# Optimization experiments

Hardware: AMD Instinct MI355X
Metric: run time of the kernel (lower is better)

The kernel has to match this reference:

```python
import jax, jax.numpy as jnp
import numpy as np

N_NODES = 50000
NUM_FEA = 213
HID, IN_HEAD = 16, 12
OUT_DIM, OUT_HEAD = 8, 8
NEG_SLOPE = 0.2


def gat_conv(x, W, att_src, att_dst, bias, src, dst, H, C):
    # x: [N, F] -> h: [N, H, C]
    N = x.shape[0]
    h = (x @ W).reshape(N, H, C)
    a_s = jnp.sum(h * att_src, axis=-1)  # [N, H]
    a_d = jnp.sum(h * att_dst, axis=-1)  # [N, H]
    e = jax.nn.leaky_relu(a_s[src] + a_d[dst], NEG_SLOPE)  # [E, H]
    # segment softmax over incoming edges of each dst node
    m = jax.ops.segment_max(e, dst, num_segments=N)
    ex = jnp.exp(e - m[dst])
    denom = jax.ops.segment_sum(ex, dst, num_segments=N)
    alpha = ex / denom[dst]  # [E, H]
    out = jax.ops.segment_sum(h[src] * alpha[:, :, None], dst, num_segments=N)
    return out.reshape(N, H * C) + bias


def setup_inputs() -> dict:
    key = jax.random.key(0)
    ks = jax.random.split(key, 16)
    E = 800000
    P = 16384
    features = jax.random.normal(ks[0], (N_NODES, NUM_FEA), dtype=jnp.float32)
    edge_index = jax.random.randint(ks[1], (2, E), 0, N_NODES, dtype=jnp.int32)
    node1_index = jax.random.randint(ks[2], (P,), 0, N_NODES, dtype=jnp.int32)
    node2_index = jax.random.randint(ks[3], (P,), 0, N_NODES, dtype=jnp.int32)
    s1 = 1.0 / np.sqrt(NUM_FEA)
    s2 = 1.0 / np.sqrt(HID * IN_HEAD)
    s3 = 1.0 / np.sqrt(OUT_DIM * OUT_HEAD * 2)
    params = {
        'W1': jax.random.normal(ks[4], (NUM_FEA, IN_HEAD * HID), jnp.float32) * s1,
        'att_src1': jax.random.normal(ks[5], (IN_HEAD, HID), jnp.float32) * s1,
        'att_dst1': jax.random.normal(ks[6], (IN_HEAD, HID), jnp.float32) * s1,
        'b1': jnp.zeros((IN_HEAD * HID,), jnp.float32),
        'W2': jax.random.normal(ks[7], (IN_HEAD * HID, OUT_HEAD * OUT_DIM), jnp.float32) * s2,
        'att_src2': jax.random.normal(ks[8], (OUT_HEAD, OUT_DIM), jnp.float32) * s2,
        'att_dst2': jax.random.normal(ks[9], (OUT_HEAD, OUT_DIM), jnp.float32) * s2,
        'b2': jnp.zeros((OUT_HEAD * OUT_DIM,), jnp.float32),
        'linW': jax.random.normal(ks[10], (OUT_DIM * OUT_HEAD * 2, 2), jnp.float32) * s3,
        'linb': jnp.zeros((2,), jnp.float32),
    }
    return dict(features=features, edge_index=edge_index,
                node1_index=node1_index, node2_index=node2_index, **params)


def reference(features, edge_index, node1_index, node2_index,
              W1, att_src1, att_dst1, b1, W2, att_src2, att_dst2, b2, linW, linb):
    # eval mode: dropout(p=0.8) is identity
    N = features.shape[0]
    self_loops = jnp.arange(N, dtype=edge_index.dtype)
    src = jnp.concatenate([edge_index[0], self_loops])
    dst = jnp.concatenate([edge_index[1], self_loops])
    x = gat_conv(features, W1, att_src1, att_dst1, b1, src, dst, IN_HEAD, HID)
    x = jax.nn.elu(x)
    x = gat_conv(x, W2, att_src2, att_dst2, b2, src, dst, OUT_HEAD, OUT_DIM)
    x = jax.nn.elu(x)
    pair = jnp.concatenate([x[node1_index], x[node2_index]], axis=1)
    y_pred = jax.nn.sigmoid(pair @ linW + linb)
    return (y_pred, x)
```

## Files before the change

### kernel.cpp

```cpp
#include <hip/hip_runtime.h>
#include <hip/hip_bf16.h>

#define HID1 16
#define NHEAD1 12
#define F1 (HID1*NHEAD1)
#define HID2 8
#define NHEAD2 8
#define F2 (HID2*NHEAD2)
#define NUM_FEA 213
#define NEG_SLOPE 0.2f
#define KP 224
#define KP2 192
#define LDK 40
#define MR1 64
#define MROWS 128
#define NC1 224
#define NW2R 80
#define SLOTS 56
#define BINS 256
#define NPB 196
#define CAP 4096
#define FILLB 256
#define EPT 13

typedef __attribute__((ext_vector_type(8))) __bf16 bf16x8;
typedef __attribute__((ext_vector_type(4))) float floatx4;
typedef __attribute__((ext_vector_type(2))) float floatx2;
typedef float floatx4u __attribute__((ext_vector_type(4), aligned(4)));
typedef unsigned short ushort_t;

static __device__ __forceinline__ unsigned short f2bf(float f) {
    unsigned u = __float_as_uint(f);
    unsigned r = (u + 0x7fffu + ((u >> 16) & 1u)) >> 16;
    return (unsigned short)r;
}
static __device__ __forceinline__ float lrelu(float e) {
    return e > 0.f ? e : NEG_SLOPE * e;
}
static __device__ __forceinline__ float elu(float v) {
    return v > 0.f ? v : (__expf(v) - 1.f);
}


__global__ __launch_bounds__(256) void prep_kernel(
        const float* __restrict__ W1, const float* __restrict__ as1w,
        const float* __restrict__ ad1w, ushort_t* __restrict__ Wt1,
        const float* __restrict__ W2, const float* __restrict__ as2w,
        const float* __restrict__ ad2w, ushort_t* __restrict__ Wt2,
        const int* __restrict__ ei, int* __restrict__ binctr,
        unsigned* __restrict__ binbuf, int E, int Etot, int nwb) {
    int b = (int)blockIdx.x;
    int tid = threadIdx.x;
    if (b >= nwb) {
        __shared__ int hist[BINS];
        __shared__ int cur[BINS];
        int fb = b - nwb;
        if (tid < BINS) hist[tid] = 0;
        __syncthreads();
        unsigned stash[EPT];
        int base_e = fb * 256 + tid;
#pragma unroll
        for (int i = 0; i < EPT; i++) {
            int e = base_e + i * (FILLB * 256);
            unsigned pk = 0xffffffffu;
            if (e < Etot) {
                int s, d;
                if (e < E) { s = ei[e]; d = ei[E + e]; } else { s = e - E; d = s; }
                pk = (unsigned)s | ((unsigned)d << 16);
                atomicAdd(&hist[(unsigned)d / NPB], 1);
            }
            stash[i] = pk;
        }
        __syncthreads();
        if (tid < BINS) cur[tid] = atomicAdd(&binctr[tid], hist[tid]);
        __syncthreads();
#pragma unroll
        for (int i = 0; i < EPT; i++) {
            unsigned pk = stash[i];
            if (pk != 0xffffffffu) {
                int d = (int)(pk >> 16);
                int bin = (int)((unsigned)d / NPB);
                int dl = d - bin * NPB;
                int r = atomicAdd(&cur[bin], 1);
                if (r < CAP)
                    binbuf[(long)bin * CAP + r] = (pk & 0xffffu) | ((unsigned)dl << 16);
            }
        }
        return;
    }
    int j = b * 256 + tid;
    if (j < NC1 * KP) {
        int n = j / KP, k = j - n * KP;
        float v = 0.f;
        if (k < NUM_FEA) {
            if (n < 192) {
                v = W1[(long)k * F1 + n];
            } else if (n < 204) {
                int hd = n - 192;
                for (int c = 0; c < HID1; c++)
                    v += W1[(long)k * F1 + hd * HID1 + c] * as1w[hd * HID1 + c];
            } else if (n < 216) {
                int hd = n - 204;
                for (int c = 0; c < HID1; c++)
                    v += W1[(long)k * F1 + hd * HID1 + c] * ad1w[hd * HID1 + c];
            }
        }
        Wt1[j] = f2bf(v);
    } else {
        int j2 = j - NC1 * KP;
        if (j2 < NW2R * KP2) {
            int n = j2 / KP2, k = j2 - n * KP2;
            float v;
            if (n < 64) {
                v = W2[(long)k * F2 + n];
            } else if (n < 72) {
                int hd = n - 64;
                v = 0.f;
                for (int c = 0; c < HID2; c++)
                    v += W2[(long)k * F2 + hd * HID2 + c] * as2w[hd * HID2 + c];
            } else {
                int hd = n - 72;
                v = 0.f;
                for (int c = 0; c < HID2; c++)
                    v += W2[(long)k * F2 + hd * HID2 + c] * ad2w[hd * HID2 + c];
            }
            Wt2[j2] = f2bf(v);
        }
    }
}


static __device__ __forceinline__ void stageA(ushort_t* dst, const float* xp,
                                              bool ok, int col) {
    union { int4 q; ushort_t u[8]; } pk;
    if (ok && col + 8 <= NUM_FEA) {
        floatx4u a = *(const floatx4u*)(xp + col);
        floatx4u c = *(const floatx4u*)(xp + col + 4);
#pragma unroll
        for (int j = 0; j < 4; j++) { pk.u[j] = f2bf(a[j]); pk.u[4 + j] = f2bf(c[j]); }
    } else {
#pragma unroll
        for (int j = 0; j < 8; j++) {
            float v = (ok && col + j < NUM_FEA) ? xp[col + j] : 0.f;
            pk.u[j] = f2bf(v);
        }
    }
    *(int4*)dst = pk.q;
}

__global__ __launch_bounds__(256) void gemm1_bs_kernel(
        const float* __restrict__ X, const ushort_t* __restrict__ Wt,
        ushort_t* __restrict__ Hout, float* __restrict__ as_, float* __restrict__ ad_,
        const unsigned* __restrict__ binbuf, const int* __restrict__ binctr,
        ushort_t* __restrict__ esrcp, int* __restrict__ cnt,
        int N, int nblk_gemm) {
    __shared__ ushort_t As[MR1 * LDK];
    __shared__ ushort_t Bs[NC1 * LDK];
    __shared__ int lcnt[NPB];
    int tid = threadIdx.x;
    if ((int)blockIdx.x >= nblk_gemm) {
        int b = (int)blockIdx.x - nblk_gemm;
        if (tid < NPB) lcnt[tid] = 0;
        __syncthreads();
        int cntb = binctr[b];
        if (cntb > CAP) cntb = CAP;
        const unsigned* seg = binbuf + (long)b * CAP;
        for (int t = tid; t < cntb; t += 256) {
            unsigned u = seg[t];
            int s = (int)(u & 0xffffu);
            int dl = (int)(u >> 16);
            int slot = atomicAdd(&lcnt[dl], 1);
            if (slot < SLOTS)
                esrcp[(long)(b * NPB + dl) * SLOTS + slot] = (ushort_t)s;
        }
        __syncthreads();
        int d = b * NPB + tid;
        if (tid < NPB && d < N) cnt[d] = lcnt[tid];
        return;
    }
    int wave = tid >> 6, lane = tid & 63;
    int q = lane >> 4, l16 = lane & 15;
    int wm = (wave >> 1) * 32;
    int wn = (wave & 1) * 112;
    long row0 = (long)blockIdx.x * MR1;

    int r0 = tid >> 2, ksl = (tid & 3) * 8;
    long gr0 = row0 + r0;
    bool ok0 = gr0 < N;
    const float* xp0 = X + gr0 * NUM_FEA;
    ushort_t* lds0 = &As[r0 * LDK + ksl];

    floatx4 acc[2][7] = {};

    for (int k0 = 0; k0 < KP; k0 += 32) {
        stageA(lds0, xp0, ok0, k0 + ksl);
#pragma unroll
        for (int p = 0; p < 4; p++) {
            int idx = p * 256 + tid;
            if (idx < NC1 * 4) {
                int r = idx >> 2, ks = (idx & 3) * 8;
                *(int4*)&Bs[r * LDK + ks] = *(const int4*)&Wt[(long)r * KP + k0 + ks];
            }
        }
        __syncthreads();
        bf16x8 af[2], bfr[7];
#pragma unroll
        for (int rt = 0; rt < 2; rt++)
            af[rt] = *(const bf16x8*)&As[(wm + rt * 16 + l16) * LDK + q * 8];
#pragma unroll
        for (int ct = 0; ct < 7; ct++)
            bfr[ct] = *(const bf16x8*)&Bs[(wn + ct * 16 + l16) * LDK + q * 8];
#pragma unroll
        for (int rt = 0; rt < 2; rt++)
#pragma unroll
            for (int ct = 0; ct < 7; ct++)
                acc[rt][ct] = __builtin_amdgcn_mfma_f32_16x16x32_bf16(af[rt], bfr[ct], acc[rt][ct], 0, 0, 0);
        __syncthreads();
    }
#pragma unroll
    for (int rt = 0; rt < 2; rt++) {
#pragma unroll
        for (int r = 0; r < 4; r++) {
            long grow = row0 + wm + rt * 16 + q * 4 + r;
            if (grow < N) {
#pragma unroll
                for (int ct = 0; ct < 7; ct++) {
                    int col = wn + ct * 16 + l16;
                    float v = acc[rt][ct][r];
                    if (col < 192)      Hout[grow * F1 + col] = f2bf(v);
                    else if (col < 204) as_[grow * NHEAD1 + col - 192] = v;
                    else if (col < 216) ad_[grow * NHEAD1 + col - 204] = v;
                }
            }
        }
    }
}


__global__ __launch_bounds__(256) void gemm2_mfma(const ushort_t* __restrict__ Xbf,
                                                  const ushort_t* __restrict__ Wt,
                                                  ushort_t* __restrict__ Hout,
                                                  float* __restrict__ as_,
                                                  float* __restrict__ ad_, int N) {
    __shared__ ushort_t As[MROWS * LDK];
    __shared__ ushort_t Bs[96 * LDK];
    int tid = threadIdx.x;
    int wave = tid >> 6, lane = tid & 63;
    int q = lane >> 4, l16 = lane & 15;
    int wm = (wave >> 1) * 64;
    int wn = (wave & 1) * 48;
    long row0 = (long)blockIdx.x * MROWS;

    floatx4 acc[4][3] = {};

    for (int k0 = 0; k0 < KP2; k0 += 32) {
#pragma unroll
        for (int p = 0; p < 2; p++) {
            int idx = p * 256 + tid;
            int r = idx >> 2, ks = (idx & 3) * 8;
            *(int4*)&As[r * LDK + ks] = *(const int4*)&Xbf[(row0 + r) * KP2 + k0 + ks];
        }
#pragma unroll
        for (int p = 0; p < 2; p++) {
            int idx = p * 256 + tid;
            if (idx < 96 * 4) {
                int r = idx >> 2, ks = (idx & 3) * 8;
                int4 z = {0, 0, 0, 0};
                *(int4*)&Bs[r * LDK + ks] = (r < NW2R) ? *(const int4*)&Wt[(long)r * KP2 + k0 + ks] : z;
            }
        }
        __syncthreads();
        bf16x8 af[4], bfr[3];
#pragma unroll
        for (int rt = 0; rt < 4; rt++)
            af[rt] = *(const bf16x8*)&As[(wm + rt * 16 + l16) * LDK + q * 8];
#pragma unroll
        for (int ct = 0; ct < 3; ct++)
            bfr[ct] = *(const bf16x8*)&Bs[(wn + ct * 16 + l16) * LDK + q * 8];
#pragma unroll
        for (int rt = 0; rt < 4; rt++)
#pragma unroll
            for (int ct = 0; ct < 3; ct++)
                acc[rt][ct] = __builtin_amdgcn_mfma_f32_16x16x32_bf16(af[rt], bfr[ct], acc[rt][ct], 0, 0, 0);
        __syncthreads();
    }
#pragma unroll
    for (int rt = 0; rt < 4; rt++) {
#pragma unroll
        for (int r = 0; r < 4; r++) {
            long grow = row0 + wm + rt * 16 + q * 4 + r;
            if (grow < N) {
#pragma unroll
                for (int ct = 0; ct < 3; ct++) {
                    int col = wn + ct * 16 + l16;
                    float v = acc[rt][ct][r];
                    if (col < 64)      Hout[grow * F2 + col] = f2bf(v);
                    else if (col < 72) as_[grow * NHEAD2 + col - 64] = v;
                    else if (col < 80) ad_[grow * NHEAD2 + col - 72] = v;
                }
            }
        }
    }
}


__global__ __launch_bounds__(256) void gather1_kernel(const int* __restrict__ cnt,
                                                      const ushort_t* __restrict__ esrcp,
                                                      const float* __restrict__ as_,
                                                      const float* __restrict__ ad_,
                                                      const ushort_t* __restrict__ h,
                                                      const float* __restrict__ bias,
                                                      ushort_t* __restrict__ xout, int N) {
    int d = blockIdx.x * 4 + (threadIdx.x >> 6);
    if (d >= N) return;
    int l = threadIdx.x & 63;
    int jc = l < 48 ? l : 47;
    int hj = jc >> 2;
    int e0 = l / 12, h0 = l - e0 * 12;
    int l64 = l + 64;
    int e1 = l64 / 12, h1 = l64 - e1 * 12;
    int deg = cnt[d]; if (deg > SLOTS) deg = SLOTS;
    int sfull = (int)esrcp[d * SLOTS + (l < SLOTS - 1 ? l : SLOTS - 1)];
    float adv0 = ad_[d * NHEAD1 + h0];
    float adv1 = ad_[d * NHEAD1 + h1];
    float4 b4 = ((const float4*)bias)[jc];
    const char* hcol = (const char*)(h + 4 * jc);

    floatx2 a01 = {0.f, 0.f}, a23 = {0.f, 0.f};
    float accd = 0.f;

    for (int p0 = 0; p0 < deg; p0 += 8) {
        int s_e[8];
#pragma unroll
        for (int i = 0; i < 8; i++) s_e[i] = __shfl(sfull, p0 + i, 64);
        uint2 g[8];
#pragma unroll
        for (int i = 0; i < 8; i++) {
            unsigned off = (unsigned)s_e[i] * (unsigned)(F1 * 2);
            g[i] = *(const uint2*)(hcol + off);
        }
        int sq0 = __shfl(sfull, p0 + e0, 64);
        int sq1 = __shfl(sfull, p0 + e1, 64);
        float a0v = as_[sq0 * NHEAD1 + h0];
        float a1v = as_[sq1 * NHEAD1 + h1];
        float w0 = (p0 + e0 < deg) ? __expf(lrelu(a0v + adv0)) : 0.f;
        float w1 = (e1 < 8 && p0 + e1 < deg) ? __expf(lrelu(a1v + adv1)) : 0.f;
#pragma unroll
        for (int i = 0; i < 8; i++) {
            float wi;
            if (i <= 4) {
                wi = __shfl(w0, i * 12 + hj, 64);
            } else if (i == 5) {
                float wa = __shfl(w0, 60 + hj, 64);
                int srcb = hj >= 4 ? hj - 4 : 0;
                float wb = __shfl(w1, srcb, 64);
                wi = (hj < 4) ? wa : wb;
            } else {
                wi = __shfl(w1, i * 12 + hj - 64, 64);
            }
            unsigned x = g[i].x, y = g[i].y;
            floatx2 h01, h23, w2;
            h01.x = __uint_as_float(x << 16);
            h01.y = __uint_as_float(x & 0xffff0000u);
            h23.x = __uint_as_float(y << 16);
            h23.y = __uint_as_float(y & 0xffff0000u);
            w2.x = wi; w2.y = wi;
            a01 += w2 * h01;
            a23 += w2 * h23;
            accd += wi;
        }
    }
    if (l < 48) {
        float inv = __builtin_amdgcn_rcpf(accd);
        float v0 = elu(a01.x * inv + b4.x);
        float v1 = elu(a01.y * inv + b4.y);
        float v2 = elu(a23.x * inv + b4.z);
        float v3 = elu(a23.y * inv + b4.w);
        uint2 outp;
        outp.x = (unsigned)f2bf(v0) | ((unsigned)f2bf(v1) << 16);
        outp.y = (unsigned)f2bf(v2) | ((unsigned)f2bf(v3) << 16);
        *(uint2*)(xout + (long)d * F1 + 4 * l) = outp;
    }
}


__global__ __launch_bounds__(256) void gather2_kernel(const int* __restrict__ cnt,
                                                      const ushort_t* __restrict__ esrcp,
                                                      const float* __restrict__ as_,
                                                      const float* __restrict__ ad_,
                                                      const ushort_t* __restrict__ h,
                                                      const float* __restrict__ bias,
                                                      float* __restrict__ xout, int N) {
    int d = blockIdx.x * 4 + (threadIdx.x >> 6);
    if (d >= N) return;
    int l = threadIdx.x & 63;
    int cg = l & 15;
    int hj = cg >> 1;
    int e_lo = l >> 4;
    int ie0 = l >> 3, hq = l & 7;
    int ie1 = 8 + ie0;
    int deg = cnt[d]; if (deg > SLOTS) deg = SLOTS;
    int sfull = (int)esrcp[d * SLOTS + (l < SLOTS - 1 ? l : SLOTS - 1)];
    float advq = ad_[d * NHEAD2 + hq];
    const char* hcol = (const char*)(h + 4 * cg);

    floatx2 a01 = {0.f, 0.f}, a23 = {0.f, 0.f};
    float accd = 0.f;

    for (int p0 = 0; p0 < deg; p0 += 16) {
        int se[4];
#pragma unroll
        for (int k = 0; k < 4; k++) se[k] = __shfl(sfull, p0 + e_lo + 4 * k, 64);
        uint2 g[4];
#pragma unroll
        for (int k = 0; k < 4; k++) {
            unsigned off = (unsigned)se[k] * (unsigned)(F2 * 2);
            g[k] = *(const uint2*)(hcol + off);
        }
        int sq0 = __shfl(sfull, p0 + ie0, 64);
        int sq1 = __shfl(sfull, p0 + ie1, 64);
        float a0v = as_[sq0 * NHEAD2 + hq];
        float a1v = as_[sq1 * NHEAD2 + hq];
        float w0d = (p0 + ie0 < deg) ? __expf(lrelu(a0v + advq)) : 0.f;
        float w1d = (p0 + ie1 < deg) ? __expf(lrelu(a1v + advq)) : 0.f;
#pragma unroll
        for (int k = 0; k < 4; k++) {
            int i = e_lo + 4 * k;
            float wk = (k < 2) ? __shfl(w0d, i * 8 + hj, 64)
                               : __shfl(w1d, i * 8 + hj - 64, 64);
            unsigned x = g[k].x, y = g[k].y;
            floatx2 h01, h23, w2;
            h01.x = __uint_as_float(x << 16);
            h01.y = __uint_as_float(x & 0xffff0000u);
            h23.x = __uint_as_float(y << 16);
            h23.y = __uint_as_float(y & 0xffff0000u);
            w2.x = wk; w2.y = wk;
            a01 += w2 * h01;
            a23 += w2 * h23;
            accd += wk;
        }
    }
    a01.x += __shfl_xor(a01.x, 16, 64); a01.x += __shfl_xor(a01.x, 32, 64);
    a01.y += __shfl_xor(a01.y, 16, 64); a01.y += __shfl_xor(a01.y, 32, 64);
    a23.x += __shfl_xor(a23.x, 16, 64); a23.x += __shfl_xor(a23.x, 32, 64);
    a23.y += __shfl_xor(a23.y, 16, 64); a23.y += __shfl_xor(a23.y, 32, 64);
    accd  += __shfl_xor(accd, 16, 64);  accd  += __shfl_xor(accd, 32, 64);
    if (l < 16) {
        float4 b4 = ((const float4*)bias)[cg];
        float inv = __builtin_amdgcn_rcpf(accd);
        float4 outp;
        outp.x = elu(a01.x * inv + b4.x);
        outp.y = elu(a01.y * inv + b4.y);
        outp.z = elu(a23.x * inv + b4.z);
        outp.w = elu(a23.y * inv + b4.w);
        *(float4*)(xout + (long)d * F2 + 4 * cg) = outp;
    }
}


__global__ void pair_kernel(const float* __restrict__ x, const int* __restrict__ n1,
                            const int* __restrict__ n2, const float* __restrict__ linW,
                            const float* __restrict__ linb, float* __restrict__ y, int P) {
    int idx = blockIdx.x * blockDim.x + threadIdx.x;
    if (idx >= P) return;
    const float4* xa = (const float4*)(x + (long)n1[idx] * F2);
    const float4* xb = (const float4*)(x + (long)n2[idx] * F2);
    float a0 = linb[0], a1 = linb[1];
#pragma unroll
    for (int k4 = 0; k4 < F2 / 4; k4++) {
        float4 v = xa[k4];
        int k = k4 * 4;
        a0 += v.x * linW[2 * k] + v.y * linW[2 * (k + 1)] + v.z * linW[2 * (k + 2)] + v.w * linW[2 * (k + 3)];
        a1 += v.x * linW[2 * k + 1] + v.y * linW[2 * (k + 1) + 1] + v.z * linW[2 * (k + 2) + 1] + v.w * linW[2 * (k + 3) + 1];
    }
#pragma unroll
    for (int k4 = 0; k4 < F2 / 4; k4++) {
        float4 v = xb[k4];
        int k = F2 + k4 * 4;
        a0 += v.x * linW[2 * k] + v.y * linW[2 * (k + 1)] + v.z * linW[2 * (k + 2)] + v.w * linW[2 * (k + 3)];
        a1 += v.x * linW[2 * k + 1] + v.y * linW[2 * (k + 1) + 1] + v.z * linW[2 * (k + 2) + 1] + v.w * linW[2 * (k + 3) + 1];
    }
    y[2 * idx]     = 1.f / (1.f + __expf(-a0));
    y[2 * idx + 1] = 1.f / (1.f + __expf(-a1));
}


extern "C" void kernel_launch(void* const* d_in, const int* in_sizes, int n_in,
                              void* d_out, int out_size, void* d_ws, size_t ws_size,
                              hipStream_t stream) {
    const float* features = (const float*)d_in[0];
    const int*   ei       = (const int*)d_in[1];
    const int*   n1       = (const int*)d_in[2];
    const int*   n2       = (const int*)d_in[3];
    const float* W1       = (const float*)d_in[4];
    const float* att_s1   = (const float*)d_in[5];
    const float* att_d1   = (const float*)d_in[6];
    const float* b1       = (const float*)d_in[7];
    const float* W2       = (const float*)d_in[8];
    const float* att_s2   = (const float*)d_in[9];
    const float* att_d2   = (const float*)d_in[10];
    const float* b2       = (const float*)d_in[11];
    const float* linW     = (const float*)d_in[12];
    const float* linb     = (const float*)d_in[13];

    const int N = in_sizes[0] / NUM_FEA;
    const int E = in_sizes[1] / 2;
    const int P = in_sizes[2];
    const int Etot = E + N;

    const int nblk1 = (N + MR1 - 1) / MR1;
    const int nblk2 = (N + MROWS - 1) / MROWS;
    const int nwb = (NC1 * KP + NW2R * KP2 + 255) / 256;

    float* ws = (float*)d_ws;
    long o = 0;
    float* h1r  = ws + o; o += (long)N * F1 / 2;
    float* x1r  = ws + o; o += (long)N * F1 / 2;
    float* as1  = ws + o; o += (long)N * NHEAD1;
    float* ad1  = ws + o; o += (long)N * NHEAD1;
    float* h2r  = ws + o; o += (long)N * F2 / 2;
    float* as2  = ws + o; o += (long)N * NHEAD2;
    float* ad2  = ws + o; o += (long)N * NHEAD2;
    float* w1r  = ws + o; o += ((long)NC1 * KP + 1) / 2;
    float* w2r  = ws + o; o += ((long)NW2R * KP2 + 1) / 2;
    float* esr  = ws + o; o += ((long)N * SLOTS + 1) / 2;
    unsigned* binbuf = (unsigned*)(ws + o); o += (long)BINS * CAP;
    int* binctr = (int*)(ws + o); o += BINS;
    int* cnt  = (int*)(ws + o); o += N;

    ushort_t* h1b   = (ushort_t*)h1r;
    ushort_t* x1bf  = (ushort_t*)x1r;
    ushort_t* h2b   = (ushort_t*)h2r;
    ushort_t* Wt1   = (ushort_t*)w1r;
    ushort_t* Wt2   = (ushort_t*)w2r;
    ushort_t* esrcp = (ushort_t*)esr;

    float* y_out = (float*)d_out;
    float* x_out = (float*)d_out + (long)2 * P;

    hipMemsetAsync(binctr, 0, (size_t)BINS * sizeof(int), stream);

    prep_kernel<<<nwb + FILLB, 256, 0, stream>>>(
        W1, att_s1, att_d1, Wt1, W2, att_s2, att_d2, Wt2,
        ei, binctr, binbuf, E, Etot, nwb);

    gemm1_bs_kernel<<<nblk1 + BINS, 256, 0, stream>>>(
        features, Wt1, h1b, as1, ad1, binbuf, binctr, esrcp, cnt, N, nblk1);

    gather1_kernel<<<(N + 3) / 4, 256, 0, stream>>>(cnt, esrcp, as1, ad1, h1b, b1, x1bf, N);

    gemm2_mfma<<<nblk2, 256, 0, stream>>>(x1bf, Wt2, h2b, as2, ad2, N);
    gather2_kernel<<<(N + 3) / 4, 256, 0, stream>>>(cnt, esrcp, as2, ad2, h2b, b2, x_out, N);

    pair_kernel<<<(P + 255) / 256, 256, 0, stream>>>(x_out, n1, n2, linW, linb, y_out, P);
}
```

Baseline: 249.9 us.

## Prefetch next K-tile of A and B into registers during gemm1 MFMA loop

The gemm1 main loop now loads the next 32-wide K slice of X and the weight tile into registers right after the barrier, so those global loads overlap the MFMA work on the current tile, then writes them to LDS at the top of the next iteration. It also retunes the fill-side blocking constants (FILLB and EPT) so each fill thread handles fewer edges across more blocks. The prefetch adds register pressure (8 floats plus 4 int4 per thread), which could reduce occupancy.

```diff
diff --git a/kernel.cpp b/kernel.cpp
--- a/kernel.cpp
+++ b/kernel.cpp
@@ -20,8 +20,8 @@
 #define BINS 256
 #define NPB 196
 #define CAP 4096
-#define FILLB 256
-#define EPT 13
+#define FILLB 512
+#define EPT 7
 
 typedef __attribute__((ext_vector_type(8))) __bf16 bf16x8;
 typedef __attribute__((ext_vector_type(4))) float floatx4;
@@ -130,21 +130,23 @@
 }
 
 
-static __device__ __forceinline__ void stageA(ushort_t* dst, const float* xp,
-                                              bool ok, int col) {
-    union { int4 q; ushort_t u[8]; } pk;
+static __device__ __forceinline__ void loadA(float* va, const float* xp,
+                                             bool ok, int col) {
     if (ok && col + 8 <= NUM_FEA) {
         floatx4u a = *(const floatx4u*)(xp + col);
         floatx4u c = *(const floatx4u*)(xp + col + 4);
 #pragma unroll
-        for (int j = 0; j < 4; j++) { pk.u[j] = f2bf(a[j]); pk.u[4 + j] = f2bf(c[j]); }
+        for (int j = 0; j < 4; j++) { va[j] = a[j]; va[4 + j] = c[j]; }
     } else {
 #pragma unroll
-        for (int j = 0; j < 8; j++) {
-            float v = (ok && col + j < NUM_FEA) ? xp[col + j] : 0.f;
-            pk.u[j] = f2bf(v);
-        }
-    }
+        for (int j = 0; j < 8; j++)
+            va[j] = (ok && col + j < NUM_FEA) ? xp[col + j] : 0.f;
+    }
+}
+static __device__ __forceinline__ void writeA(ushort_t* dst, const float* va) {
+    union { int4 q; ushort_t u[8]; } pk;
+#pragma unroll
+    for (int j = 0; j < 8; j++) pk.u[j] = f2bf(va[j]);
     *(int4*)dst = pk.q;
 }
 
@@ -189,20 +191,36 @@
     bool ok0 = gr0 < N;
     const float* xp0 = X + gr0 * NUM_FEA;
     ushort_t* lds0 = &As[r0 * LDK + ksl];
+    int br[4], bks[4];
+    bool bok[4];
+#pragma unroll
+    for (int p = 0; p < 4; p++) {
+        int idx = p * 256 + tid;
+        bok[p] = idx < NC1 * 4;
+        br[p] = idx >> 2; bks[p] = (idx & 3) * 8;
+    }
 
     floatx4 acc[2][7] = {};
+    float va[8];
+    int4 vb[4];
+
+    loadA(va, xp0, ok0, ksl);
+#pragma unroll
+    for (int p = 0; p < 4; p++)
+        if (bok[p]) vb[p] = *(const int4*)&Wt[(long)br[p] * KP + bks[p]];
 
     for (int k0 = 0; k0 < KP; k0 += 32) {
-        stageA(lds0, xp0, ok0, k0 + ksl);
-#pragma unroll
-        for (int p = 0; p < 4; p++) {
-            int idx = p * 256 + tid;
-            if (idx < NC1 * 4) {
-                int r = idx >> 2, ks = (idx & 3) * 8;
-                *(int4*)&Bs[r * LDK + ks] = *(const int4*)&Wt[(long)r * KP + k0 + ks];
-            }
-        }
-        __syncthreads();
+        writeA(lds0, va);
+#pragma unroll
+        for (int p = 0; p < 4; p++)
+            if (bok[p]) *(int4*)&Bs[br[p] * LDK + bks[p]] = vb[p];
+        __syncthreads();
+        if (k0 + 32 < KP) {
+            loadA(va, xp0, ok0, k0 + 32 + ksl);
+#pragma unroll
+            for (int p = 0; p < 4; p++)
+                if (bok[p]) vb[p] = *(const int4*)&Wt[(long)br[p] * KP + k0 + 32 + bks[p]];
+        }
         bf16x8 af[2], bfr[7];
 #pragma unroll
         for (int rt = 0; rt < 2; rt++)
```

After: 270.8 us. +8.3%, slower.
